# Kernel tuning notes

Hardware: AMD Instinct MI355X
Metric: run time of the kernel (lower is better)

The kernel has to match this reference:

```python
import jax, jax.numpy as jnp
import numpy as np

N_EXPERTS = 64
TOPK = 4
DIM = 2048
B_T = 8192


def setup_inputs() -> dict:
    key = jax.random.key(0)
    k1, k2 = jax.random.split(key)
    x = jax.random.normal(k1, (B_T, DIM), jnp.float32)
    W = jax.random.normal(k2, (N_EXPERTS, DIM), jnp.float32) * 0.02  # nn.Linear weight (out, in)
    router_bias = jnp.zeros((N_EXPERTS,), jnp.float32)  # registered buffer, init zeros
    return {"x": x, "W": W, "router_bias": router_bias, "token_capacity": 3072}


def _route(x, W, router_bias, token_capacity):
    """Faithful serial greedy capacity-aware routing.

    Replicates the torch nested loop (k-major, token-minor order):
      - per step, pick argmax over the token's (mutated) logits among experts
        with remaining capacity;
      - full experts whose logit exceeds the chosen one get permanently set
        to -inf in that token's logit row (exactly what the inner while-style
        loop does);
      - if no expert has capacity, selected stays -1, weight 0, and the whole
        row becomes -inf (torch sets the top expert to -inf n_experts times).
    """
    logits0 = x @ W.T + router_bias                       # (N, E)
    scores = jax.nn.softmax(logits0, axis=-1)             # (N, E)
    cap = token_capacity // TOPK                          # python int
    remaining0 = jnp.full((N_EXPERTS,), float(cap), jnp.float32)
    N = x.shape[0]
    NEG = jnp.float32(-jnp.inf)

    def step(carry, i):
        logits, remaining = carry
        b = i % N                                         # token index (k-major order)
        row = logits[b]                                   # (E,)
        masked = jnp.where(remaining > 0, row, NEG)
        chosen = jnp.argmax(masked)
        ok = remaining[chosen] > 0                        # False only if all experts full
        sel = jnp.where(ok, chosen, -1).astype(jnp.int32)
        w = jnp.where(ok, scores[b, chosen], jnp.float32(0.0))
        full = remaining <= 0
        cval = row[chosen]
        # full experts 'above' the chosen one were visited and zapped to -inf
        new_row = jnp.where(ok,
                            jnp.where(full & (row > cval), NEG, row),
                            jnp.full_like(row, NEG))
        logits = logits.at[b].set(new_row)
        remaining = remaining.at[chosen].add(jnp.where(ok, jnp.float32(-1.0), jnp.float32(0.0)))
        return (logits, remaining), (sel, w)

    (_, _), (sel_f, w_f) = jax.lax.scan(step, (logits0, remaining0),
                                        jnp.arange(TOPK * N))
    selected = sel_f.reshape(TOPK, N).T                   # (N, TOPK)
    weights = w_f.reshape(TOPK, N).T                      # (N, TOPK)
    weights = weights / (weights.sum(axis=-1, keepdims=True) + 1e-8)
    return selected, weights


def reference(x, W, router_bias, token_capacity):
    return _route(x, W, router_bias, token_capacity)
```

## Files before the change

### kernel.cpp

```cpp
#include <hip/hip_runtime.h>
#include <math.h>

#define N_TOK 8192
#define DIM   2048
#define NE    64
#define TOPK  4
#define THETA 2e-3f
#define TPB2  16
#define NBLK  (N_TOK / TPB2)
#define RSTR  260
#define HSTR  16

typedef short bf16x8 __attribute__((ext_vector_type(8)));
typedef float f32x4  __attribute__((ext_vector_type(4)));

#define OFF_LOGITS 0
#define OFF_MAXV   (OFF_LOGITS + N_TOK * NE)
#define OFF_DENOM  (OFF_MAXV + N_TOK)
#define OFF_W1     (OFF_DENOM + N_TOK)
#define OFF_C1     (OFF_W1 + N_TOK)
#define OFF_HIST   (OFF_C1 + N_TOK)
#define OFF_WH     (OFF_HIST + NE * HSTR)
#define OFF_WL     (OFF_WH + NE * DIM / 2)
#define OFF_WT     (OFF_WL + NE * DIM / 2)
#define OFF_WTMP   (OFF_WT + NE * DIM)

__device__ inline void cvt2(float a, float b, unsigned& hi, unsigned& lo) {
    const unsigned ua = __float_as_uint(a), ub = __float_as_uint(b);
    hi = __builtin_amdgcn_perm(ub, ua, 0x07060302u);
    const float ra = a - __uint_as_float(ua & 0xFFFF0000u);
    const float rb = b - __uint_as_float(ub & 0xFFFF0000u);
    lo = __builtin_amdgcn_perm(__float_as_uint(rb), __float_as_uint(ra), 0x07060302u);
}

union FragU { unsigned u[4]; bf16x8 v; uint4 q; };

__device__ inline void make_frags(const float4& p, const float4& q,
                                  bf16x8& hi, bf16x8& lo) {
    FragU H, L;
    cvt2(p.x, p.y, H.u[0], L.u[0]);
    cvt2(p.z, p.w, H.u[1], L.u[1]);
    cvt2(q.x, q.y, H.u[2], L.u[2]);
    cvt2(q.z, q.w, H.u[3], L.u[3]);
    hi = H.v; lo = L.v;
}

__global__ __launch_bounds__(256)
void k_wc(const float* __restrict__ W, unsigned short* __restrict__ wh2,
          unsigned short* __restrict__ wl2, float* __restrict__ wt,
          int* __restrict__ hist) {
    const int t = blockIdx.x * 256 + threadIdx.x;
    if (t < NE * HSTR) hist[t] = 0;
    const int l  = t & 63;
    const int grp = t >> 6;
    const int nt = grp & 3;
    const int kc = grp >> 2;
    const int e  = nt * 16 + (l & 15);
    const int k0 = kc * 32 + (l >> 4) * 8;

    const float4 p = *reinterpret_cast<const float4*>(W + (size_t)e * DIM + k0);
    const float4 q = *reinterpret_cast<const float4*>(W + (size_t)e * DIM + k0 + 4);
    FragU H, L;
    cvt2(p.x, p.y, H.u[0], L.u[0]);
    cvt2(p.z, p.w, H.u[1], L.u[1]);
    cvt2(q.x, q.y, H.u[2], L.u[2]);
    cvt2(q.z, q.w, H.u[3], L.u[3]);
    const size_t off = (size_t)grp * 512 + l * 8;
    *reinterpret_cast<uint4*>(wh2 + off) = H.q;
    *reinterpret_cast<uint4*>(wl2 + off) = L.q;

    wt[(size_t)(k0 + 0) * NE + e] = p.x;
    wt[(size_t)(k0 + 1) * NE + e] = p.y;
    wt[(size_t)(k0 + 2) * NE + e] = p.z;
    wt[(size_t)(k0 + 3) * NE + e] = p.w;
    wt[(size_t)(k0 + 4) * NE + e] = q.x;
    wt[(size_t)(k0 + 5) * NE + e] = q.y;
    wt[(size_t)(k0 + 6) * NE + e] = q.z;
    wt[(size_t)(k0 + 7) * NE + e] = q.w;
}

__global__ __launch_bounds__(512, 4)
void k_main(const float* __restrict__ x, const unsigned short* __restrict__ wh2,
            const unsigned short* __restrict__ wl2, const float* __restrict__ bias,
            const float* __restrict__ wt,
            float* __restrict__ logits, float* __restrict__ maxv,
            float* __restrict__ denomv, float* __restrict__ w1f,
            int* __restrict__ c1, int* __restrict__ hist) {
    __shared__ __align__(16) float xs[2][TPB2 * RSTR];
    __shared__ float red[8][TPB2][68];
    __shared__ float lbuf[TPB2][68];
    __shared__ int   selS[TPB2];
    __shared__ short flagIdx[TPB2];
    __shared__ int   flagCnt;

    const int tid = threadIdx.x;
    const int w   = tid >> 6;
    const int l   = tid & 63;
    const int t0  = blockIdx.x * TPB2;
    const int m   = l & 15;
    const int g   = l >> 4;

    if (tid == 0) flagCnt = 0;

    const float* xrow0 = x + (size_t)(t0 + 2 * w) * DIM + l * 4;
    const float* xrow1 = x + (size_t)(t0 + 2 * w + 1) * DIM + l * 4;
    float* st0 = &xs[0][(2 * w) * RSTR + l * 4];
    float* st1 = &xs[0][(2 * w + 1) * RSTR + l * 4];
    const int xs1off = TPB2 * RSTR;

    const unsigned short* bh = wh2 + (size_t)w * 2048 + l * 8;
    const unsigned short* bl = wl2 + (size_t)w * 2048 + l * 8;

    f32x4 accA[4], accB[4];
    #pragma unroll
    for (int nt = 0; nt < 4; ++nt)
        #pragma unroll
        for (int r = 0; r < 4; ++r) { accA[nt][r] = 0.0f; accB[nt][r] = 0.0f; }

    {
        const float4 r0 = *reinterpret_cast<const float4*>(xrow0);
        const float4 r1 = *reinterpret_cast<const float4*>(xrow1);
        *reinterpret_cast<float4*>(st0) = r0;
        *reinterpret_cast<float4*>(st1) = r1;
    }
    uint4 BH[2][4], BL[2][4];
    #pragma unroll
    for (int nt = 0; nt < 4; ++nt) {
        BH[0][nt] = *reinterpret_cast<const uint4*>(bh + nt * 512);
        BL[0][nt] = *reinterpret_cast<const uint4*>(bl + nt * 512);
    }
    __syncthreads();

    const int aoff = m * RSTR + w * 32 + g * 8;

    #pragma unroll
    for (int win = 0; win < 8; ++win) {
        const int cur = win & 1, nxt = cur ^ 1;
        float4 nx0, nx1;
        if (win < 7) {
            nx0 = *reinterpret_cast<const float4*>(xrow0 + (win + 1) * 256);
            nx1 = *reinterpret_cast<const float4*>(xrow1 + (win + 1) * 256);
            #pragma unroll
            for (int nt = 0; nt < 4; ++nt) {
                BH[nxt][nt] = *reinterpret_cast<const uint4*>(
                    bh + (size_t)(win + 1) * 16384 + nt * 512);
                BL[nxt][nt] = *reinterpret_cast<const uint4*>(
                    bl + (size_t)(win + 1) * 16384 + nt * 512);
            }
        }

        const float4 p = *reinterpret_cast<const float4*>(&xs[0][cur * xs1off + aoff]);
        const float4 q = *reinterpret_cast<const float4*>(&xs[0][cur * xs1off + aoff + 4]);
        bf16x8 ah, al;
        make_frags(p, q, ah, al);

        #pragma unroll
        for (int nt = 0; nt < 4; ++nt) {
            FragU b; b.q = BH[cur][nt];
            accA[nt] = __builtin_amdgcn_mfma_f32_16x16x32_bf16(ah, b.v, accA[nt], 0, 0, 0);
            accB[nt] = __builtin_amdgcn_mfma_f32_16x16x32_bf16(al, b.v, accB[nt], 0, 0, 0);
        }
        #pragma unroll
        for (int nt = 0; nt < 4; ++nt) {
            FragU b; b.q = BL[cur][nt];
            accB[nt] = __builtin_amdgcn_mfma_f32_16x16x32_bf16(ah, b.v, accB[nt], 0, 0, 0);
        }

        if (win < 7) {
            *reinterpret_cast<float4*>(st0 + nxt * xs1off) = nx0;
            *reinterpret_cast<float4*>(st1 + nxt * xs1off) = nx1;
        }
        __syncthreads();
    }

    #pragma unroll
    for (int nt = 0; nt < 4; ++nt)
        #pragma unroll
        for (int r = 0; r < 4; ++r)
            red[w][g * 4 + r][nt * 16 + m] = accA[nt][r] + accB[nt][r];
    __syncthreads();

    for (int e2 = tid; e2 < TPB2 * NE; e2 += 512) {
        const int t = e2 >> 6, e = e2 & 63;
        float s = red[0][t][e];
        #pragma unroll
        for (int ww = 1; ww < 8; ++ww) s += red[ww][t][e];
        s += bias[e];
        logits[(size_t)(t0 + t) * NE + e] = s;
        lbuf[t][e] = s;
    }
    __syncthreads();

    #pragma unroll
    for (int tt = 0; tt < 2; ++tt) {
        const int t = w * 2 + tt;
        const float lv = lbuf[t][l];
        float v1 = lv; int i1 = l; float v2 = -INFINITY;
        #pragma unroll
        for (int off = 32; off; off >>= 1) {
            const float ov1 = __shfl_xor(v1, off);
            const int   oi1 = __shfl_xor(i1, off);
            const float ov2 = __shfl_xor(v2, off);
            if (ov1 > v1 || (ov1 == v1 && oi1 < i1)) {
                v2 = fmaxf(v1, ov2); v1 = ov1; i1 = oi1;
            } else {
                v2 = fmaxf(v2, ov1);
            }
        }
        float s = expf(lv - v1);
        #pragma unroll
        for (int off = 32; off; off >>= 1) s += __shfl_xor(s, off);
        if (l == 0) {
            const int row = t0 + t;
            maxv[row]   = v1;
            denomv[row] = s;
            c1[row]     = i1;
            w1f[row]    = 1.0f / s;
            selS[t]     = i1;
            if (v1 - v2 < THETA) {
                const int ix = atomicAdd(&flagCnt, 1);
                flagIdx[ix] = (short)t;
            }
        }
    }
    __syncthreads();

    const int nf = flagCnt;
    for (int fi = 0; fi < nf; ++fi) {
        const int tl  = flagIdx[fi];
        const int row = t0 + tl;
        const float* xr = x + (size_t)row * DIM + w * 256;
        const float* wb = wt + (size_t)(w * 256) * NE + l;
        float a0 = 0.0f, a1 = 0.0f;
        #pragma unroll 4
        for (int k = 0; k < 256; k += 8) {
            const float4 x0 = *reinterpret_cast<const float4*>(xr + k);
            const float4 x1 = *reinterpret_cast<const float4*>(xr + k + 4);
            a0 = fmaf(x0.x, wb[(size_t)(k + 0) * NE], a0);
            a0 = fmaf(x0.y, wb[(size_t)(k + 1) * NE], a0);
            a0 = fmaf(x0.z, wb[(size_t)(k + 2) * NE], a0);
            a0 = fmaf(x0.w, wb[(size_t)(k + 3) * NE], a0);
            a1 = fmaf(x1.x, wb[(size_t)(k + 4) * NE], a1);
            a1 = fmaf(x1.y, wb[(size_t)(k + 5) * NE], a1);
            a1 = fmaf(x1.z, wb[(size_t)(k + 6) * NE], a1);
            a1 = fmaf(x1.w, wb[(size_t)(k + 7) * NE], a1);
        }
        red[w][0][l] = a0 + a1;
        __syncthreads();
        if (w == 0) {
            float lg = bias[l];
            #pragma unroll
            for (int s2 = 0; s2 < 8; ++s2) lg += red[s2][0][l];
            logits[(size_t)row * NE + l] = lg;
            float v = lg; int idx = l;
            #pragma unroll
            for (int off = 32; off; off >>= 1) {
                const float ov = __shfl_xor(v, off);
                const int   oi = __shfl_xor(idx, off);
                if (ov > v || (ov == v && oi < idx)) { v = ov; idx = oi; }
            }
            float p = expf(lg - v);
            #pragma unroll
            for (int off = 32; off; off >>= 1) p += __shfl_xor(p, off);
            if (l == 0) {
                maxv[row]   = v;
                denomv[row] = p;
                c1[row]     = idx;
                w1f[row]    = 1.0f / p;
                selS[tl]    = idx;
            }
        }
        __syncthreads();
    }

    if (w == 0) {
        int cnt = 0;
        #pragma unroll
        for (int t = 0; t < TPB2; ++t) cnt += (selS[t] == l) ? 1 : 0;
        if (cnt) atomicAdd(&hist[l * HSTR], cnt);
    }
}

__global__ __launch_bounds__(256)
void k_decide(const int* __restrict__ hist, const int* __restrict__ c1,
              const float* __restrict__ w1, const float* __restrict__ logits,
              const float* __restrict__ maxv, const float* __restrict__ denomv,
              const int* __restrict__ tc, float* __restrict__ out,
              float* __restrict__ wtmp) {
    __shared__ int flagS;
    const int tid = threadIdx.x;
    const int cap = tc[0] / TOPK;
    if (tid < NE) {
        const bool bad = (TOPK * hist[tid * HSTR] > cap);
        const unsigned long long mm = __ballot(bad);
        if (tid == 0) flagS = (mm == 0ull) ? 1 : 0;
    }
    __syncthreads();

    if (flagS) {
        const int b = blockIdx.x * 256 + tid;
        const float se = (float)c1[b];
        const float wv = w1[b];
        const float wn = wv / (4.0f * wv + 1e-8f);
        *reinterpret_cast<float4*>(out + (size_t)b * 4) = make_float4(se, se, se, se);
        *reinterpret_cast<float4*>(out + (size_t)N_TOK * TOPK + (size_t)b * 4) =
            make_float4(wn, wn, wn, wn);
        return;
    }

    if (blockIdx.x != 0) return;
    if (tid < 64) {
        const int e = tid;
        int rem = cap;
        for (int k = 0; k < TOPK; ++k) {
            for (int b = 0; b < N_TOK; ++b) {
                const float lg = logits[(size_t)b * NE + e];
                float v = (rem > 0) ? lg : -INFINITY;
                int idx = e;
                #pragma unroll
                for (int off = 32; off; off >>= 1) {
                    const float ov = __shfl_xor(v, off);
                    const int   oi = __shfl_xor(idx, off);
                    if (ov > v || (ov == v && oi < idx)) { v = ov; idx = oi; }
                }
                const bool ok = (v != -INFINITY);
                if (ok && e == idx) rem -= 1;
                const float lc = __shfl(lg, idx);
                if (e == 0) {
                    out[(size_t)b * TOPK + k]  = ok ? (float)idx : -1.0f;
                    wtmp[(size_t)b * TOPK + k] = ok ? expf(lc - maxv[b]) / denomv[b] : 0.0f;
                }
            }
        }
    }
    __syncthreads();
    for (int b = tid; b < N_TOK; b += 256) {
        const float w0 = wtmp[b * 4 + 0], w1_ = wtmp[b * 4 + 1];
        const float w2 = wtmp[b * 4 + 2], w3 = wtmp[b * 4 + 3];
        const float s = ((w0 + w1_) + w2) + w3 + 1e-8f;
        out[N_TOK * TOPK + b * 4 + 0] = w0 / s;
        out[N_TOK * TOPK + b * 4 + 1] = w1_ / s;
        out[N_TOK * TOPK + b * 4 + 2] = w2 / s;
        out[N_TOK * TOPK + b * 4 + 3] = w3 / s;
    }
}

extern "C" void kernel_launch(void* const* d_in, const int* in_sizes, int n_in,
                              void* d_out, int out_size, void* d_ws, size_t ws_size,
                              hipStream_t stream) {
    const float* x    = (const float*)d_in[0];
    const float* W    = (const float*)d_in[1];
    const float* bias = (const float*)d_in[2];
    const int*   tc   = (const int*)d_in[3];

    float* ws       = (float*)d_ws;
    float* logits   = ws + OFF_LOGITS;
    float* maxv     = ws + OFF_MAXV;
    float* denomv   = ws + OFF_DENOM;
    float* w1f      = ws + OFF_W1;
    int*   c1       = (int*)(ws + OFF_C1);
    int*   hist     = (int*)(ws + OFF_HIST);
    unsigned short* wh2 = (unsigned short*)(ws + OFF_WH);
    unsigned short* wl2 = (unsigned short*)(ws + OFF_WL);
    float* wt       = ws + OFF_WT;
    float* wtmp     = ws + OFF_WTMP;
    float* out      = (float*)d_out;

    k_wc<<<NE * DIM / 8 / 256, 256, 0, stream>>>(W, wh2, wl2, wt, hist);
    k_main<<<NBLK, 512, 0, stream>>>(x, wh2, wl2, bias, wt, logits, maxv, denomv,
                                     w1f, c1, hist);
    k_decide<<<N_TOK / 256, 256, 0, stream>>>(hist, c1, w1f, logits, maxv, denomv,
                                              tc, out, wtmp);
}
```

Baseline: 131.3 us.

## Load x and W directly into MFMA fragments, double tokens per block, fuse output write

The main kernel no longer stages x through shared memory or reads pre-split bf16 weight copies. Each lane now loads its fp32 x and W fragments straight from global memory and splits them into hi/lo bf16 in registers. Each block handles 32 tokens instead of 16, so every W fragment is reused across two token tiles, and the per-loop __syncthreads are removed. The fast-path output write moves from the decide kernel into the main kernel, which drops the c1/w1 workspace round trip, and the decide kernel now launches as a single block. The cost is W conversion repeated in every block, more registers per thread (occupancy hint lowered to 2), and uncoalesced strided global loads.

```diff
diff --git a/kernel.cpp b/kernel.cpp
--- a/kernel.cpp
+++ b/kernel.cpp
@@ -6,9 +6,8 @@
 #define NE    64
 #define TOPK  4
 #define THETA 2e-3f
-#define TPB2  16
-#define NBLK  (N_TOK / TPB2)
-#define RSTR  260
+#define TPB   32
+#define NBLK  (N_TOK / TPB)
 #define HSTR  16
 
 typedef short bf16x8 __attribute__((ext_vector_type(8)));
@@ -17,12 +16,8 @@
 #define OFF_LOGITS 0
 #define OFF_MAXV   (OFF_LOGITS + N_TOK * NE)
 #define OFF_DENOM  (OFF_MAXV + N_TOK)
-#define OFF_W1     (OFF_DENOM + N_TOK)
-#define OFF_C1     (OFF_W1 + N_TOK)
-#define OFF_HIST   (OFF_C1 + N_TOK)
-#define OFF_WH     (OFF_HIST + NE * HSTR)
-#define OFF_WL     (OFF_WH + NE * DIM / 2)
-#define OFF_WT     (OFF_WL + NE * DIM / 2)
+#define OFF_HIST   (OFF_DENOM + N_TOK)
+#define OFF_WT     (OFF_HIST + NE * HSTR)
 #define OFF_WTMP   (OFF_WT + NE * DIM)
 
 __device__ inline void cvt2(float a, float b, unsigned& hi, unsigned& lo) {
@@ -46,8 +41,7 @@
 }
 
 __global__ __launch_bounds__(256)
-void k_wc(const float* __restrict__ W, unsigned short* __restrict__ wh2,
-          unsigned short* __restrict__ wl2, float* __restrict__ wt,
+void k_wc(const float* __restrict__ W, float* __restrict__ wt,
           int* __restrict__ hist) {
     const int t = blockIdx.x * 256 + threadIdx.x;
     if (t < NE * HSTR) hist[t] = 0;
@@ -60,15 +54,6 @@
 
     const float4 p = *reinterpret_cast<const float4*>(W + (size_t)e * DIM + k0);
     const float4 q = *reinterpret_cast<const float4*>(W + (size_t)e * DIM + k0 + 4);
-    FragU H, L;
-    cvt2(p.x, p.y, H.u[0], L.u[0]);
-    cvt2(p.z, p.w, H.u[1], L.u[1]);
-    cvt2(q.x, q.y, H.u[2], L.u[2]);
-    cvt2(q.z, q.w, H.u[3], L.u[3]);
-    const size_t off = (size_t)grp * 512 + l * 8;
-    *reinterpret_cast<uint4*>(wh2 + off) = H.q;
-    *reinterpret_cast<uint4*>(wl2 + off) = L.q;
-
     wt[(size_t)(k0 + 0) * NE + e] = p.x;
     wt[(size_t)(k0 + 1) * NE + e] = p.y;
     wt[(size_t)(k0 + 2) * NE + e] = p.z;
@@ -79,108 +64,99 @@
     wt[(size_t)(k0 + 7) * NE + e] = q.w;
 }
 
-__global__ __launch_bounds__(512, 4)
-void k_main(const float* __restrict__ x, const unsigned short* __restrict__ wh2,
-            const unsigned short* __restrict__ wl2, const float* __restrict__ bias,
-            const float* __restrict__ wt,
+__global__ __launch_bounds__(512, 2)
+void k_main(const float* __restrict__ x, const float* __restrict__ W,
+            const float* __restrict__ bias, const float* __restrict__ wt,
             float* __restrict__ logits, float* __restrict__ maxv,
-            float* __restrict__ denomv, float* __restrict__ w1f,
-            int* __restrict__ c1, int* __restrict__ hist) {
-    __shared__ __align__(16) float xs[2][TPB2 * RSTR];
-    __shared__ float red[8][TPB2][68];
-    __shared__ float lbuf[TPB2][68];
-    __shared__ int   selS[TPB2];
-    __shared__ short flagIdx[TPB2];
+            float* __restrict__ denomv, int* __restrict__ hist,
+            float* __restrict__ out) {
+    __shared__ float red[8][TPB][68];
+    __shared__ float lbuf[TPB][68];
+    __shared__ int   selS[TPB];
+    __shared__ float wS[TPB];
+    __shared__ short flagIdx[TPB];
     __shared__ int   flagCnt;
 
     const int tid = threadIdx.x;
     const int w   = tid >> 6;
     const int l   = tid & 63;
-    const int t0  = blockIdx.x * TPB2;
+    const int t0  = blockIdx.x * TPB;
     const int m   = l & 15;
     const int g   = l >> 4;
 
     if (tid == 0) flagCnt = 0;
 
-    const float* xrow0 = x + (size_t)(t0 + 2 * w) * DIM + l * 4;
-    const float* xrow1 = x + (size_t)(t0 + 2 * w + 1) * DIM + l * 4;
-    float* st0 = &xs[0][(2 * w) * RSTR + l * 4];
-    float* st1 = &xs[0][(2 * w + 1) * RSTR + l * 4];
-    const int xs1off = TPB2 * RSTR;
-
-    const unsigned short* bh = wh2 + (size_t)w * 2048 + l * 8;
-    const unsigned short* bl = wl2 + (size_t)w * 2048 + l * 8;
-
-    f32x4 accA[4], accB[4];
-    #pragma unroll
-    for (int nt = 0; nt < 4; ++nt)
-        #pragma unroll
-        for (int r = 0; r < 4; ++r) { accA[nt][r] = 0.0f; accB[nt][r] = 0.0f; }
-
-    {
-        const float4 r0 = *reinterpret_cast<const float4*>(xrow0);
-        const float4 r1 = *reinterpret_cast<const float4*>(xrow1);
-        *reinterpret_cast<float4*>(st0) = r0;
-        *reinterpret_cast<float4*>(st1) = r1;
-    }
-    uint4 BH[2][4], BL[2][4];
+    const float* aP0 = x + (size_t)(t0 + m) * DIM + w * 32 + g * 8;
+    const float* aP1 = aP0 + (size_t)16 * DIM;
+    const float* bP  = W + (size_t)m * DIM + w * 32 + g * 8;
+
+    f32x4 accA[2][4], accB[2][4];
+    #pragma unroll
+    for (int t = 0; t < 2; ++t)
+        #pragma unroll
+        for (int nt = 0; nt < 4; ++nt)
+            #pragma unroll
+            for (int r = 0; r < 4; ++r) { accA[t][nt][r] = 0.0f; accB[t][nt][r] = 0.0f; }
+
+    float4 cA[2][4], cB[2][8];
+    cA[0][0] = *reinterpret_cast<const float4*>(aP0);
+    cA[0][1] = *reinterpret_cast<const float4*>(aP0 + 4);
+    cA[0][2] = *reinterpret_cast<const float4*>(aP1);
+    cA[0][3] = *reinterpret_cast<const float4*>(aP1 + 4);
     #pragma unroll
     for (int nt = 0; nt < 4; ++nt) {
-        BH[0][nt] = *reinterpret_cast<const uint4*>(bh + nt * 512);
-        BL[0][nt] = *reinterpret_cast<const uint4*>(bl + nt * 512);
-    }
-    __syncthreads();
-
-    const int aoff = m * RSTR + w * 32 + g * 8;
+        cB[0][nt * 2 + 0] = *reinterpret_cast<const float4*>(bP + (size_t)nt * 16 * DIM);
+        cB[0][nt * 2 + 1] = *reinterpret_cast<const float4*>(bP + (size_t)nt * 16 * DIM + 4);
+    }
 
     #pragma unroll
     for (int win = 0; win < 8; ++win) {
         const int cur = win & 1, nxt = cur ^ 1;
-        float4 nx0, nx1;
         if (win < 7) {
-            nx0 = *reinterpret_cast<const float4*>(xrow0 + (win + 1) * 256);
-            nx1 = *reinterpret_cast<const float4*>(xrow1 + (win + 1) * 256);
+            const int ko = (win + 1) * 256;
+            cA[nxt][0] = *reinterpret_cast<const float4*>(aP0 + ko);
+            cA[nxt][1] = *reinterpret_cast<const float4*>(aP0 + ko + 4);
+            cA[nxt][2] = *reinterpret_cast<const float4*>(aP1 + ko);
+            cA[nxt][3] = *reinterpret_cast<const float4*>(aP1 + ko + 4);
             #pragma unroll
             for (int nt = 0; nt < 4; ++nt) {
-                BH[nxt][nt] = *reinterpret_cast<const uint4*>(
-                    bh + (size_t)(win + 1) * 16384 + nt * 512);
-                BL[nxt][nt] = *reinterpret_cast<const uint4*>(
-                    bl + (size_t)(win + 1) * 16384 + nt * 512);
-            }
-        }
-
-        const float4 p = *reinterpret_cast<const float4*>(&xs[0][cur * xs1off + aoff]);
-        const float4 q = *reinterpret_cast<const float4*>(&xs[0][cur * xs1off + aoff + 4]);
-        bf16x8 ah, al;
-        make_frags(p, q, ah, al);
-
-        #pragma unroll
-        for (int nt = 0; nt < 4; ++nt) {
-            FragU b; b.q = BH[cur][nt];
-            accA[nt] = __builtin_amdgcn_mfma_f32_16x16x32_bf16(ah, b.v, accA[nt], 0, 0, 0);
-            accB[nt] = __builtin_amdgcn_mfma_f32_16x16x32_bf16(al, b.v, accB[nt], 0, 0, 0);
-        }
-        #pragma unroll
-        for (int nt = 0; nt < 4; ++nt) {
-            FragU b; b.q = BL[cur][nt];
-            accB[nt] = __builtin_amdgcn_mfma_f32_16x16x32_bf16(ah, b.v, accB[nt], 0, 0, 0);
-        }
-
-        if (win < 7) {
-            *reinterpret_cast<float4*>(st0 + nxt * xs1off) = nx0;
-            *reinterpret_cast<float4*>(st1 + nxt * xs1off) = nx1;
-        }
-        __syncthreads();
-    }
-
-    #pragma unroll
-    for (int nt = 0; nt < 4; ++nt)
-        #pragma unroll
-        for (int r = 0; r < 4; ++r)
-            red[w][g * 4 + r][nt * 16 + m] = accA[nt][r] + accB[nt][r];
-    __syncthreads();
-
-    for (int e2 = tid; e2 < TPB2 * NE; e2 += 512) {
+                cB[nxt][nt * 2 + 0] =
+                    *reinterpret_cast<const float4*>(bP + (size_t)nt * 16 * DIM + ko);
+                cB[nxt][nt * 2 + 1] =
+                    *reinterpret_cast<const float4*>(bP + (size_t)nt * 16 * DIM + ko + 4);
+            }
+        }
+
+        bf16x8 bh[4], bl[4];
+        #pragma unroll
+        for (int nt = 0; nt < 4; ++nt)
+            make_frags(cB[cur][nt * 2], cB[cur][nt * 2 + 1], bh[nt], bl[nt]);
+
+        #pragma unroll
+        for (int t = 0; t < 2; ++t) {
+            bf16x8 ah, al;
+            make_frags(cA[cur][t * 2], cA[cur][t * 2 + 1], ah, al);
+            #pragma unroll
+            for (int nt = 0; nt < 4; ++nt) {
+                accA[t][nt] = __builtin_amdgcn_mfma_f32_16x16x32_bf16(ah, bh[nt], accA[t][nt], 0, 0, 0);
+                accB[t][nt] = __builtin_amdgcn_mfma_f32_16x16x32_bf16(al, bh[nt], accB[t][nt], 0, 0, 0);
+            }
+            #pragma unroll
+            for (int nt = 0; nt < 4; ++nt)
+                accB[t][nt] = __builtin_amdgcn_mfma_f32_16x16x32_bf16(ah, bl[nt], accB[t][nt], 0, 0, 0);
+        }
+    }
+
+    #pragma unroll
+    for (int t = 0; t < 2; ++t)
+        #pragma unroll
+        for (int nt = 0; nt < 4; ++nt)
+            #pragma unroll
+            for (int r = 0; r < 4; ++r)
+                red[w][t * 16 + g * 4 + r][nt * 16 + m] = accA[t][nt][r] + accB[t][nt][r];
+    __syncthreads();
+
+    for (int e2 = tid; e2 < TPB * NE; e2 += 512) {
         const int t = e2 >> 6, e = e2 & 63;
         float s = red[0][t][e];
         #pragma unroll
@@ -192,8 +168,8 @@
     __syncthreads();
 
     #pragma unroll
-    for (int tt = 0; tt < 2; ++tt) {
-        const int t = w * 2 + tt;
+    for (int tt = 0; tt < 4; ++tt) {
+        const int t = w * 4 + tt;
         const float lv = lbuf[t][l];
         float v1 = lv; int i1 = l; float v2 = -INFINITY;
         #pragma unroll
@@ -214,9 +190,8 @@
             const int row = t0 + t;
             maxv[row]   = v1;
             denomv[row] = s;
-            c1[row]     = i1;
-            w1f[row]    = 1.0f / s;
             selS[t]     = i1;
+            wS[t]       = 1.0f / s;
             if (v1 - v2 < THETA) {
                 const int ix = atomicAdd(&flagCnt, 1);
                 flagIdx[ix] = (short)t;
@@ -265,9 +240,8 @@
             if (l == 0) {
                 maxv[row]   = v;
                 denomv[row] = p;
-                c1[row]     = idx;
-                w1f[row]    = 1.0f / p;
                 selS[tl]    = idx;
+                wS[tl]      = 1.0f / p;
             }
         }
         __syncthreads();
@@ -276,14 +250,23 @@
     if (w == 0) {
         int cnt = 0;
         #pragma unroll
-        for (int t = 0; t < TPB2; ++t) cnt += (selS[t] == l) ? 1 : 0;
+        for (int t = 0; t < TPB; ++t) cnt += (selS[t] == l) ? 1 : 0;
         if (cnt) atomicAdd(&hist[l * HSTR], cnt);
     }
+
+    if (tid < TPB) {
+        const int row = t0 + tid;
+        const float se = (float)selS[tid];
+        const float wv = wS[tid];
+        const float wn = wv / (4.0f * wv + 1e-8f);
+        *reinterpret_cast<float4*>(out + (size_t)row * 4) = make_float4(se, se, se, se);
+        *reinterpret_cast<float4*>(out + (size_t)N_TOK * TOPK + (size_t)row * 4) =
+            make_float4(wn, wn, wn, wn);
+    }
 }
 
 __global__ __launch_bounds__(256)
-void k_decide(const int* __restrict__ hist, const int* __restrict__ c1,
-              const float* __restrict__ w1, const float* __restrict__ logits,
+void k_decide(const int* __restrict__ hist, const float* __restrict__ logits,
               const float* __restrict__ maxv, const float* __restrict__ denomv,
               const int* __restrict__ tc, float* __restrict__ out,
               float* __restrict__ wtmp) {
@@ -296,19 +279,8 @@
         if (tid == 0) flagS = (mm == 0ull) ? 1 : 0;
     }
     __syncthreads();
-
-    if (flagS) {
-        const int b = blockIdx.x * 256 + tid;
-        const float se = (float)c1[b];
-        const float wv = w1[b];
-        const float wn = wv / (4.0f * wv + 1e-8f);
-        *reinterpret_cast<float4*>(out + (size_t)b * 4) = make_float4(se, se, se, se);
-        *reinterpret_cast<float4*>(out + (size_t)N_TOK * TOPK + (size_t)b * 4) =
-            make_float4(wn, wn, wn, wn);
-        return;
-    }
-
-    if (blockIdx.x != 0) return;
+    if (flagS) return;
+
     if (tid < 64) {
         const int e = tid;
         int rem = cap;
@@ -357,18 +329,13 @@
     float* logits   = ws + OFF_LOGITS;
     float* maxv     = ws + OFF_MAXV;
     float* denomv   = ws + OFF_DENOM;
-    float* w1f      = ws + OFF_W1;
-    int*   c1       = (int*)(ws + OFF_C1);
     int*   hist     = (int*)(ws + OFF_HIST);
-    unsigned short* wh2 = (unsigned short*)(ws + OFF_WH);
-    unsigned short* wl2 = (unsigned short*)(ws + OFF_WL);
     float* wt       = ws + OFF_WT;
     float* wtmp     = ws + OFF_WTMP;
     float* out      = (float*)d_out;
 
-    k_wc<<<NE * DIM / 8 / 256, 256, 0, stream>>>(W, wh2, wl2, wt, hist);
-    k_main<<<NBLK, 512, 0, stream>>>(x, wh2, wl2, bias, wt, logits, maxv, denomv,
-                                     w1f, c1, hist);
-    k_decide<<<N_TOK / 256, 256, 0, stream>>>(hist, c1, w1f, logits, maxv, denomv,
-                                              tc, out, wtmp);
-}
+    k_wc<<<NE * DIM / 8 / 256, 256, 0, stream>>>(W, wt, hist);
+    k_main<<<NBLK, 512, 0, stream>>>(x, W, bias, wt, logits, maxv, denomv,
+                                     hist, out);
+    k_decide<<<1, 256, 0, stream>>>(hist, logits, maxv, denomv, tc, out, wtmp);
+}
```

Result: slower. 149.2 us (+13.6%).
